# Performance work log

Measured on AMD Instinct MI355X. Metric: run time of the kernel, lower is better.

## Reference

```python
import jax, jax.numpy as jnp
import numpy as np
import math

H = 8
E = 512
D_K = E // H
NEG = -1000000000.0
# last (and only surviving) row of dist_bar: one threshold per head
DIST_BAR = np.array([0.2, 0.3, 0.4, 0.5, 0.6, 0.7, 0.8, 0.9], dtype=np.float32)


def setup_inputs() -> dict:
    key = jax.random.key(0)
    ks = jax.random.split(key, 12)
    B, N = 8, 1024
    s = 1.0 / math.sqrt(E)
    inp = {
        "query": jax.random.normal(ks[0], (B, N, E), jnp.float32),
        "key": jax.random.normal(ks[1], (B, N, E), jnp.float32),
        "value": jax.random.normal(ks[2], (B, N, E), jnp.float32),
        "dist": jax.random.uniform(ks[3], (B, 1, N, N), jnp.float32),
        "mask": jnp.ones((B, N, N), jnp.int32),
        "Wq": jax.random.normal(ks[4], (E, E), jnp.float32) * s,
        "bq": jnp.zeros((E,), jnp.float32),
        "Wk": jax.random.normal(ks[5], (E, E), jnp.float32) * s,
        "bk": jnp.zeros((E,), jnp.float32),
        "Wv": jax.random.normal(ks[6], (E, E), jnp.float32) * s,
        "bv": jnp.zeros((E,), jnp.float32),
        "Wo": jax.random.normal(ks[7], (E, E), jnp.float32) * s,
        "bo": jnp.zeros((E,), jnp.float32),
    }
    return inp


def reference(query, key, value, dist, mask, Wq, bq, Wk, bk, Wv, bv, Wo, bo):
    B, N, _ = query.shape
    # project and split heads: [B, H, N, D_K]
    def heads(x, W, b):
        return (x @ W.T + b).reshape(B, N, H, D_K).transpose(0, 2, 1, 3)
    q = heads(query, Wq, bq)
    k = heads(key, Wk, bk)
    v = heads(value, Wv, bv)
    scores = jnp.einsum("bhqd,bhkd->bhqk", q, k) / math.sqrt(D_K)
    # padding mask: [B,N,N] -> [B,1,N,N]
    scores = jnp.where(mask[:, None, :, :] == 0, NEG, scores)
    # per-head distance mask: dist [B,1,N,N] < thr[h] -> [B,H,N,N]
    thr = jnp.asarray(DIST_BAR)[None, :, None, None]
    dmask = dist < thr
    # first row/col (global atom) always attend
    dmask = dmask.at[:, :, 0, :].set(True).at[:, :, :, 0].set(True)
    scores = jnp.where(dmask, scores, NEG)
    p = jax.nn.softmax(scores, axis=-1)
    out = jnp.einsum("bhqk,bhkd->bhqd", p, v)  # [B,H,N,D_K]
    out = out.transpose(0, 2, 1, 3).reshape(B, N, H * D_K)
    return out @ Wo.T + bo
```

## Files before the change

kernel.cpp:

```cpp
#include <hip/hip_runtime.h>
#include <stdint.h>


typedef __attribute__((ext_vector_type(8))) short short8;
typedef __attribute__((ext_vector_type(4))) float floatx4;

#define MFMA16(a, b, c) __builtin_amdgcn_mfma_f32_16x16x32_bf16((a), (b), (c), 0, 0, 0)

static __device__ __forceinline__ unsigned short f2bf(float f) {
  union { float f; unsigned u; } v; v.f = f;
  unsigned r = v.u + 0x7fffu + ((v.u >> 16) & 1u);
  return (unsigned short)(r >> 16);
}

static __device__ __forceinline__ void gload_lds16(const void* g, void* l) {
  __builtin_amdgcn_global_load_lds((const __attribute__((address_space(1))) unsigned int*)g,
                                   (__attribute__((address_space(3))) unsigned int*)l,
                                   16, 0, 0);
}
static __device__ __forceinline__ int xsw(int row) { return (row & 3) ^ ((row >> 2) & 3); }

__global__ void wcast_kernel(const float* __restrict__ Wq, const float* __restrict__ Wk,
                             const float* __restrict__ Wv, const float* __restrict__ Wo,
                             unsigned short* __restrict__ o0, unsigned short* __restrict__ o1,
                             unsigned short* __restrict__ o2, unsigned short* __restrict__ o3) {
  int i = blockIdx.x * blockDim.x + threadIdx.x;
  int w = i >> 16, loc = i & 65535;
  const float* s = (w == 0) ? Wq : (w == 1) ? Wk : (w == 2) ? Wv : Wo;
  unsigned short* d = (w == 0) ? o0 : (w == 1) ? o1 : (w == 2) ? o2 : o3;
  float4 v = ((const float4*)s)[loc];
  ushort4 o;
  o.x = f2bf(v.x); o.y = f2bf(v.y); o.z = f2bf(v.z); o.w = f2bf(v.w);
  ((ushort4*)d)[loc] = o;
}

__global__ void codes_kernel(const float* __restrict__ dist, const int* __restrict__ mask,
                             unsigned char* __restrict__ codes) {
  int t = blockIdx.x * blockDim.x + threadIdx.x;
  int flat = t << 2;
  int rem = flat & ((1 << 20) - 1);
  int i = rem >> 10;
  int j0 = rem & 1023;
  float4 d4 = ((const float4*)dist)[t];
  int4 m4 = ((const int4*)mask)[t];
  float dv[4] = {d4.x, d4.y, d4.z, d4.w};
  int mv[4] = {m4.x, m4.y, m4.z, m4.w};
  unsigned char cv[4];
#pragma unroll
  for (int u = 0; u < 4; u++) {
    float d = dv[u];
    int hmin = (d >= 0.2f) + (d >= 0.3f) + (d >= 0.4f) + (d >= 0.5f) +
               (d >= 0.6f) + (d >= 0.7f) + (d >= 0.8f) + (d >= 0.9f);
    unsigned char cc = (unsigned char)hmin;
    if (i == 0 || (j0 + u) == 0) cc = 0;
    if (mv[u] == 0) cc = 9;
    cv[u] = cc;
  }
  uchar4 o; o.x = cv[0]; o.y = cv[1]; o.z = cv[2]; o.w = cv[3];
  ((uchar4*)codes)[t] = o;
}

__global__ __launch_bounds__(256) void qkv_gemm(
    const float* __restrict__ Aq, const float* __restrict__ Ak, const float* __restrict__ Av,
    const unsigned short* __restrict__ Wqp, const unsigned short* __restrict__ Wkp,
    const unsigned short* __restrict__ Wvp,
    const float* __restrict__ bq, const float* __restrict__ bk, const float* __restrict__ bv,
    unsigned short* __restrict__ Qh, unsigned short* __restrict__ Kh,
    unsigned short* __restrict__ Vt) {
  const int z = blockIdx.z;
  const float* A = (z == 0) ? Aq : (z == 1) ? Ak : Av;
  const unsigned short* W = (z == 0) ? Wqp : (z == 1) ? Wkp : Wvp;
  const float* bias = (z == 0) ? bq : (z == 1) ? bk : bv;
  unsigned short* O = (z == 0) ? Qh : (z == 1) ? Kh : Vt;

  __shared__ __align__(16) short As[64 * 40];
  __shared__ __align__(16) short Bs[128 * 32];
  const int tid = threadIdx.x;
  const int lane = tid & 63;
  const int wave = tid >> 6;
  const int c = lane & 15;
  const int q = lane >> 4;
  const int m0 = blockIdx.x * 64;
  const int n0 = blockIdx.y * 128;
  const int wr = (wave >> 1) * 32;
  const int wc = (wave & 1) * 64;

  floatx4 acc[2][4];
#pragma unroll
  for (int i = 0; i < 2; i++)
#pragma unroll
    for (int j = 0; j < 4; j++) acc[i][j] = (floatx4)(0.0f);

  const int arow = tid >> 2, ach = tid & 3;
  const float* Ab = A + (size_t)(m0 + arow) * 512 + ach * 8;

  for (int k0 = 0; k0 < 512; k0 += 32) {
    __syncthreads();
#pragma unroll
    for (int it = 0; it < 2; it++) {
      int slot = wave * 128 + it * 64 + lane;
      int brow = slot >> 2, bch = slot & 3;
      int g = bch ^ xsw(brow);
      gload_lds16(W + (size_t)(n0 + brow) * 512 + k0 + g * 8,
                  &Bs[(size_t)(wave * 128 + it * 64) * 8]);
    }
    float4 a0 = *(const float4*)(Ab + k0);
    float4 a1 = *(const float4*)(Ab + k0 + 4);
    short8 av;
    av[0] = (short)f2bf(a0.x); av[1] = (short)f2bf(a0.y);
    av[2] = (short)f2bf(a0.z); av[3] = (short)f2bf(a0.w);
    av[4] = (short)f2bf(a1.x); av[5] = (short)f2bf(a1.y);
    av[6] = (short)f2bf(a1.z); av[7] = (short)f2bf(a1.w);
    *(short8*)(&As[arow * 40 + ach * 8]) = av;
    __syncthreads();

    short8 af[2], bfv[4];
#pragma unroll
    for (int i = 0; i < 2; i++)
      af[i] = *(const short8*)(&As[(wr + i * 16 + c) * 40 + q * 8]);
#pragma unroll
    for (int j = 0; j < 4; j++) {
      int row = wc + j * 16 + c;
      bfv[j] = *(const short8*)(&Bs[row * 32 + (q ^ xsw(row)) * 8]);
    }
#pragma unroll
    for (int i = 0; i < 2; i++)
#pragma unroll
      for (int j = 0; j < 4; j++)
        acc[i][j] = MFMA16(af[i], bfv[j], acc[i][j]);
  }

#pragma unroll
  for (int i = 0; i < 2; i++) {
    int gm0 = m0 + wr + i * 16 + q * 4;
#pragma unroll
    for (int j = 0; j < 4; j++) {
      int gn = n0 + wc + j * 16 + c;
      float bb = bias[gn];
      int h = gn >> 6, d = gn & 63;
      if (z == 2) {
        int b = gm0 >> 10, n = gm0 & 1023;
        ushort4 pk;
#pragma unroll
        for (int r = 0; r < 4; r++) pk[r] = f2bf(acc[i][j][r] + bb);
        *(ushort4*)(&Vt[(((size_t)(b * 8 + h) * 64 + d) << 10) + n]) = pk;
      } else {
#pragma unroll
        for (int r = 0; r < 4; r++) {
          int m = gm0 + r;
          int b = m >> 10, n = m & 1023;
          O[((((size_t)(b * 8 + h)) << 10) + n) * 64 + d] = f2bf(acc[i][j][r] + bb);
        }
      }
    }
  }
}

__global__ __launch_bounds__(256) void out_gemm(const unsigned short* __restrict__ A,
                                                const unsigned short* __restrict__ W,
                                                const float* __restrict__ bias,
                                                float* __restrict__ Out) {
  __shared__ __align__(16) short As[64 * 32];
  __shared__ __align__(16) short Bs[128 * 32];
  const int tid = threadIdx.x;
  const int lane = tid & 63;
  const int wave = tid >> 6;
  const int c = lane & 15;
  const int q = lane >> 4;
  const int m0 = blockIdx.x * 64;
  const int n0 = blockIdx.y * 128;
  const int wr = (wave >> 1) * 32;
  const int wc = (wave & 1) * 64;

  floatx4 acc[2][4];
#pragma unroll
  for (int i = 0; i < 2; i++)
#pragma unroll
    for (int j = 0; j < 4; j++) acc[i][j] = (floatx4)(0.0f);

  for (int k0 = 0; k0 < 512; k0 += 32) {
    __syncthreads();
    {
      int slot = wave * 64 + lane;
      int arow = slot >> 2, ach = slot & 3;
      int g = ach ^ xsw(arow);
      gload_lds16(A + (size_t)(m0 + arow) * 512 + k0 + g * 8, &As[(size_t)(wave * 64) * 8]);
    }
#pragma unroll
    for (int it = 0; it < 2; it++) {
      int slot = wave * 128 + it * 64 + lane;
      int brow = slot >> 2, bch = slot & 3;
      int g = bch ^ xsw(brow);
      gload_lds16(W + (size_t)(n0 + brow) * 512 + k0 + g * 8,
                  &Bs[(size_t)(wave * 128 + it * 64) * 8]);
    }
    __syncthreads();

    short8 af[2], bfv[4];
#pragma unroll
    for (int i = 0; i < 2; i++) {
      int row = wr + i * 16 + c;
      af[i] = *(const short8*)(&As[row * 32 + (q ^ xsw(row)) * 8]);
    }
#pragma unroll
    for (int j = 0; j < 4; j++) {
      int row = wc + j * 16 + c;
      bfv[j] = *(const short8*)(&Bs[row * 32 + (q ^ xsw(row)) * 8]);
    }
#pragma unroll
    for (int i = 0; i < 2; i++)
#pragma unroll
      for (int j = 0; j < 4; j++)
        acc[i][j] = MFMA16(af[i], bfv[j], acc[i][j]);
  }

#pragma unroll
  for (int i = 0; i < 2; i++) {
    int gm0 = m0 + wr + i * 16 + q * 4;
#pragma unroll
    for (int j = 0; j < 4; j++) {
      int gn = n0 + wc + j * 16 + c;
      float bb = bias[gn];
#pragma unroll
      for (int r = 0; r < 4; r++)
        Out[(size_t)(gm0 + r) * 512 + gn] = acc[i][j][r] + bb;
    }
  }
}

__global__ __launch_bounds__(256) void attn_kernel(const unsigned short* __restrict__ Qh,
                                                   const unsigned short* __restrict__ Kh,
                                                   const unsigned short* __restrict__ Vt,
                                                   const unsigned char* __restrict__ codes,
                                                   unsigned short* __restrict__ AO) {
  __shared__ __align__(16) unsigned short P[32 * 136];
  __shared__ __align__(16) unsigned char Ct[32 * 128];
  __shared__ float S4[4][32];
  const int tid = threadIdx.x;
  const int lane = tid & 63;
  const int wave = tid >> 6;
  const int c = lane & 15;
  const int q = lane >> 4;
  const int qt = blockIdx.x;
  const int bh = blockIdx.y;
  const int b = bh >> 3;
  const int h = bh & 7;
  const size_t base = (size_t)bh << 16;
  const int ri = wave >> 1;
  const int dh = wave & 1;

  short8 aq[2][2];
#pragma unroll
  for (int qs = 0; qs < 2; qs++)
#pragma unroll
    for (int kk = 0; kk < 2; kk++)
      aq[qs][kk] = *(const short8*)(Qh + base + (size_t)(qt * 32 + qs * 16 + c) * 64 + kk * 32 + q * 8);

  const unsigned char* cbt = codes + ((size_t)b << 20) + ((size_t)(qt * 32 + (tid >> 3)) << 10) + (tid & 7) * 16;
  const unsigned short* Vb = Vt + base;

  float rs[2][4];
#pragma unroll
  for (int qs = 0; qs < 2; qs++)
#pragma unroll
    for (int r = 0; r < 4; r++) rs[qs][r] = 0.0f;
  floatx4 o[2];
  o[0] = (floatx4)(0.0f); o[1] = (floatx4)(0.0f);

  for (int kt = 0; kt < 8; kt++) {
    uint4 cw = *(const uint4*)(cbt + kt * 128);
    const int col0 = kt * 128 + wave * 32;
    floatx4 s[2][2];
#pragma unroll
    for (int qs = 0; qs < 2; qs++)
#pragma unroll
      for (int ci = 0; ci < 2; ci++) s[qs][ci] = (floatx4)(0.0f);
#pragma unroll
    for (int ci = 0; ci < 2; ci++)
#pragma unroll
      for (int kk = 0; kk < 2; kk++) {
        short8 bk = *(const short8*)(Kh + base + (size_t)(col0 + ci * 16 + c) * 64 + kk * 32 + q * 8);
        s[0][ci] = MFMA16(aq[0][kk], bk, s[0][ci]);
        s[1][ci] = MFMA16(aq[1][kk], bk, s[1][ci]);
      }
    *(uint4*)(&Ct[(tid >> 3) * 128 + (tid & 7) * 16]) = cw;
    __syncthreads();

#pragma unroll
    for (int qs = 0; qs < 2; qs++) {
      int rowb = qs * 16 + q * 4;
#pragma unroll
      for (int ci = 0; ci < 2; ci++) {
        int colw = wave * 32 + ci * 16 + c;
#pragma unroll
        for (int r = 0; r < 4; r++) {
          int row = rowb + r;
          unsigned char code = Ct[row * 128 + colw];
          float e = (h >= (int)code) ? exp2f(s[qs][ci][r] * 0.1803368801111362f) : 0.0f;
          rs[qs][r] += e;
          P[row * 136 + colw] = f2bf(e);
        }
      }
    }
    __syncthreads();

#pragma unroll
    for (int ch = 0; ch < 4; ch++) {
      short8 ap = *(const short8*)(&P[(ri * 16 + c) * 136 + ch * 32 + q * 8]);
      short8 bv0 = *(const short8*)(Vb + (size_t)(dh * 32 + c) * 1024 + kt * 128 + ch * 32 + q * 8);
      short8 bv1 = *(const short8*)(Vb + (size_t)(dh * 32 + 16 + c) * 1024 + kt * 128 + ch * 32 + q * 8);
      o[0] = MFMA16(ap, bv0, o[0]);
      o[1] = MFMA16(ap, bv1, o[1]);
    }
  }

#pragma unroll
  for (int qs = 0; qs < 2; qs++)
#pragma unroll
    for (int r = 0; r < 4; r++) {
      float v = rs[qs][r];
      v += __shfl_xor(v, 1); v += __shfl_xor(v, 2);
      v += __shfl_xor(v, 4); v += __shfl_xor(v, 8);
      rs[qs][r] = v;
    }
  if (c == 0) {
#pragma unroll
    for (int qs = 0; qs < 2; qs++)
#pragma unroll
      for (int r = 0; r < 4; r++) S4[wave][qs * 16 + q * 4 + r] = rs[qs][r];
  }
  __syncthreads();
  float inv[4];
#pragma unroll
  for (int r = 0; r < 4; r++) {
    int row = ri * 16 + q * 4 + r;
    inv[r] = 1.0f / (S4[0][row] + S4[1][row] + S4[2][row] + S4[3][row]);
  }
#pragma unroll
  for (int r = 0; r < 4; r++) {
    int ig = qt * 32 + ri * 16 + q * 4 + r;
    size_t ob = ((size_t)((b << 10) + ig)) * 512 + h * 64 + dh * 32;
    AO[ob + c] = f2bf(o[0][r] * inv[r]);
    AO[ob + 16 + c] = f2bf(o[1][r] * inv[r]);
  }
}

extern "C" void kernel_launch(void* const* d_in, const int* in_sizes, int n_in,
                              void* d_out, int out_size, void* d_ws, size_t ws_size,
                              hipStream_t stream) {
  const float* query = (const float*)d_in[0];
  const float* key_  = (const float*)d_in[1];
  const float* value = (const float*)d_in[2];
  const float* dist  = (const float*)d_in[3];
  const int*   mask  = (const int*)d_in[4];
  const float* Wq = (const float*)d_in[5];
  const float* bq = (const float*)d_in[6];
  const float* Wk = (const float*)d_in[7];
  const float* bk = (const float*)d_in[8];
  const float* Wv = (const float*)d_in[9];
  const float* bv = (const float*)d_in[10];
  const float* Wo = (const float*)d_in[11];
  const float* bo = (const float*)d_in[12];

  char* ws = (char*)d_ws;
  size_t off = 0;
  auto alloc = [&](size_t bytes) -> char* {
    char* p = ws + off;
    off += (bytes + 255) & ~(size_t)255;
    return p;
  };
  const size_t NQKV = 8192ull * 512;
  unsigned short* wq16 = (unsigned short*)alloc(512ull * 512 * 2);
  unsigned short* wk16 = (unsigned short*)alloc(512ull * 512 * 2);
  unsigned short* wv16 = (unsigned short*)alloc(512ull * 512 * 2);
  unsigned short* wo16 = (unsigned short*)alloc(512ull * 512 * 2);
  unsigned short* Qh = (unsigned short*)alloc(NQKV * 2);
  unsigned short* Kh = (unsigned short*)alloc(NQKV * 2);
  unsigned short* Vt = (unsigned short*)alloc(NQKV * 2);
  unsigned short* AO = (unsigned short*)alloc(NQKV * 2);
  unsigned char*  codes = (unsigned char*)alloc(8ull * 1024 * 1024);

  wcast_kernel<<<1024, 256, 0, stream>>>(Wq, Wk, Wv, Wo, wq16, wk16, wv16, wo16);
  codes_kernel<<<8192, 256, 0, stream>>>(dist, mask, codes);
  qkv_gemm<<<dim3(128, 4, 3), 256, 0, stream>>>(query, key_, value, wq16, wk16, wv16,
                                                bq, bk, bv, Qh, Kh, Vt);
  attn_kernel<<<dim3(32, 64), 256, 0, stream>>>(Qh, Kh, Vt, codes, AO);
  out_gemm<<<dim3(128, 4), 256, 0, stream>>>(AO, wo16, bo, (float*)d_out);
}
```

Measured before the change: 305.5 us.

## Give each wave its own query rows and pre-permute mask codes into MFMA lane layout

```diff
diff --git a/kernel.cpp b/kernel.cpp
--- a/kernel.cpp
+++ b/kernel.cpp
@@ -35,29 +35,36 @@
 }
 
 __global__ void codes_kernel(const float* __restrict__ dist, const int* __restrict__ mask,
-                             unsigned char* __restrict__ codes) {
+                             unsigned char* __restrict__ codesP) {
   int t = blockIdx.x * blockDim.x + threadIdx.x;
   int flat = t << 2;
+  int b = flat >> 20;
   int rem = flat & ((1 << 20) - 1);
-  int i = rem >> 10;
-  int j0 = rem & 1023;
+  int row = rem >> 10;
+  int col0 = rem & 1023;
   float4 d4 = ((const float4*)dist)[t];
   int4 m4 = ((const int4*)mask)[t];
   float dv[4] = {d4.x, d4.y, d4.z, d4.w};
   int mv[4] = {m4.x, m4.y, m4.z, m4.w};
-  unsigned char cv[4];
+  int rg = row >> 5;
+  int st = (row >> 4) & 1;
+  int qq = (row >> 2) & 3;
+  int r = row & 3;
+  size_t rowbase = (size_t)(b * 32 + rg) * 32768;
+  int sub = st * 32 + r;
 #pragma unroll
   for (int u = 0; u < 4; u++) {
+    int col = col0 + u;
     float d = dv[u];
     int hmin = (d >= 0.2f) + (d >= 0.3f) + (d >= 0.4f) + (d >= 0.5f) +
                (d >= 0.6f) + (d >= 0.7f) + (d >= 0.8f) + (d >= 0.9f);
     unsigned char cc = (unsigned char)hmin;
-    if (i == 0 || (j0 + u) == 0) cc = 0;
+    if (row == 0 || col == 0) cc = 0;
     if (mv[u] == 0) cc = 9;
-    cv[u] = cc;
-  }
-  uchar4 o; o.x = cv[0]; o.y = cv[1]; o.z = cv[2]; o.w = cv[3];
-  ((uchar4*)codes)[t] = o;
+    int kt = col >> 7, ci = (col >> 4) & 7, c = col & 15;
+    int lane = qq * 16 + c;
+    codesP[rowbase + (size_t)kt * 4096 + lane * 64 + sub + ci * 4] = cc;
+  }
 }
 
 __global__ __launch_bounds__(256) void qkv_gemm(
@@ -231,118 +238,109 @@
 __global__ __launch_bounds__(256) void attn_kernel(const unsigned short* __restrict__ Qh,
                                                    const unsigned short* __restrict__ Kh,
                                                    const unsigned short* __restrict__ Vt,
-                                                   const unsigned char* __restrict__ codes,
+                                                   const unsigned char* __restrict__ codesP,
                                                    unsigned short* __restrict__ AO) {
-  __shared__ __align__(16) unsigned short P[32 * 136];
-  __shared__ __align__(16) unsigned char Ct[32 * 128];
-  __shared__ float S4[4][32];
+  __shared__ __align__(16) unsigned short P[4][32 * 132];
   const int tid = threadIdx.x;
   const int lane = tid & 63;
   const int wave = tid >> 6;
   const int c = lane & 15;
   const int q = lane >> 4;
-  const int qt = blockIdx.x;
   const int bh = blockIdx.y;
   const int b = bh >> 3;
   const int h = bh & 7;
   const size_t base = (size_t)bh << 16;
-  const int ri = wave >> 1;
-  const int dh = wave & 1;
+  const int rbase = blockIdx.x * 128 + wave * 32;
+  const int rg = rbase >> 5;
+  unsigned short* Pw = &P[wave][0];
 
   short8 aq[2][2];
 #pragma unroll
-  for (int qs = 0; qs < 2; qs++)
+  for (int st = 0; st < 2; st++)
 #pragma unroll
     for (int kk = 0; kk < 2; kk++)
-      aq[qs][kk] = *(const short8*)(Qh + base + (size_t)(qt * 32 + qs * 16 + c) * 64 + kk * 32 + q * 8);
-
-  const unsigned char* cbt = codes + ((size_t)b << 20) + ((size_t)(qt * 32 + (tid >> 3)) << 10) + (tid & 7) * 16;
+      aq[st][kk] = *(const short8*)(Qh + base + (size_t)(rbase + st * 16 + c) * 64 + kk * 32 + q * 8);
+
+  const unsigned char* cbt = codesP + (size_t)(b * 32 + rg) * 32768 + lane * 64;
+  const unsigned short* Kb = Kh + base;
   const unsigned short* Vb = Vt + base;
 
   float rs[2][4];
 #pragma unroll
-  for (int qs = 0; qs < 2; qs++)
-#pragma unroll
-    for (int r = 0; r < 4; r++) rs[qs][r] = 0.0f;
-  floatx4 o[2];
-  o[0] = (floatx4)(0.0f); o[1] = (floatx4)(0.0f);
+  for (int st = 0; st < 2; st++)
+#pragma unroll
+    for (int r = 0; r < 4; r++) rs[st][r] = 0.0f;
+  floatx4 o[2][4];
+#pragma unroll
+  for (int st = 0; st < 2; st++)
+#pragma unroll
+    for (int ci = 0; ci < 4; ci++) o[st][ci] = (floatx4)(0.0f);
 
   for (int kt = 0; kt < 8; kt++) {
-    uint4 cw = *(const uint4*)(cbt + kt * 128);
-    const int col0 = kt * 128 + wave * 32;
-    floatx4 s[2][2];
-#pragma unroll
-    for (int qs = 0; qs < 2; qs++)
-#pragma unroll
-      for (int ci = 0; ci < 2; ci++) s[qs][ci] = (floatx4)(0.0f);
-#pragma unroll
-    for (int ci = 0; ci < 2; ci++)
+    const unsigned short* Kt = Kb + (size_t)kt * 128 * 64;
+    floatx4 s[2][8];
+#pragma unroll
+    for (int ci = 0; ci < 8; ci++) { s[0][ci] = (floatx4)(0.0f); s[1][ci] = (floatx4)(0.0f); }
+#pragma unroll
+    for (int ci = 0; ci < 8; ci++)
 #pragma unroll
       for (int kk = 0; kk < 2; kk++) {
-        short8 bk = *(const short8*)(Kh + base + (size_t)(col0 + ci * 16 + c) * 64 + kk * 32 + q * 8);
+        short8 bk = *(const short8*)(Kt + (size_t)(ci * 16 + c) * 64 + kk * 32 + q * 8);
         s[0][ci] = MFMA16(aq[0][kk], bk, s[0][ci]);
         s[1][ci] = MFMA16(aq[1][kk], bk, s[1][ci]);
       }
-    *(uint4*)(&Ct[(tid >> 3) * 128 + (tid & 7) * 16]) = cw;
-    __syncthreads();
-
-#pragma unroll
-    for (int qs = 0; qs < 2; qs++) {
-      int rowb = qs * 16 + q * 4;
-#pragma unroll
-      for (int ci = 0; ci < 2; ci++) {
-        int colw = wave * 32 + ci * 16 + c;
+    const unsigned char* cp = cbt + (size_t)kt * 4096;
+    uint4 w0 = *(const uint4*)(cp);
+    uint4 w1 = *(const uint4*)(cp + 16);
+    uint4 w2 = *(const uint4*)(cp + 32);
+    uint4 w3 = *(const uint4*)(cp + 48);
+    unsigned cv[16] = {w0.x, w0.y, w0.z, w0.w, w1.x, w1.y, w1.z, w1.w,
+                       w2.x, w2.y, w2.z, w2.w, w3.x, w3.y, w3.z, w3.w};
+#pragma unroll
+    for (int st = 0; st < 2; st++)
+#pragma unroll
+      for (int ci = 0; ci < 8; ci++)
 #pragma unroll
         for (int r = 0; r < 4; r++) {
-          int row = rowb + r;
-          unsigned char code = Ct[row * 128 + colw];
-          float e = (h >= (int)code) ? exp2f(s[qs][ci][r] * 0.1803368801111362f) : 0.0f;
-          rs[qs][r] += e;
-          P[row * 136 + colw] = f2bf(e);
+          int bidx = st * 32 + ci * 4 + r;
+          int code = (cv[bidx >> 2] >> ((bidx & 3) * 8)) & 0xff;
+          float e = (h >= code) ? exp2f(s[st][ci][r] * 0.1803368801111362f) : 0.0f;
+          rs[st][r] += e;
+          Pw[(st * 16 + q * 4 + r) * 132 + ci * 16 + c] = f2bf(e);
         }
+#pragma unroll
+    for (int ch = 0; ch < 4; ch++) {
+      short8 ap0 = *(const short8*)(&Pw[(size_t)c * 132 + ch * 32 + q * 8]);
+      short8 ap1 = *(const short8*)(&Pw[(size_t)(16 + c) * 132 + ch * 32 + q * 8]);
+#pragma unroll
+      for (int ci = 0; ci < 4; ci++) {
+        short8 bv = *(const short8*)(Vb + (size_t)(ci * 16 + c) * 1024 + kt * 128 + ch * 32 + q * 8);
+        o[0][ci] = MFMA16(ap0, bv, o[0][ci]);
+        o[1][ci] = MFMA16(ap1, bv, o[1][ci]);
       }
     }
-    __syncthreads();
-
-#pragma unroll
-    for (int ch = 0; ch < 4; ch++) {
-      short8 ap = *(const short8*)(&P[(ri * 16 + c) * 136 + ch * 32 + q * 8]);
-      short8 bv0 = *(const short8*)(Vb + (size_t)(dh * 32 + c) * 1024 + kt * 128 + ch * 32 + q * 8);
-      short8 bv1 = *(const short8*)(Vb + (size_t)(dh * 32 + 16 + c) * 1024 + kt * 128 + ch * 32 + q * 8);
-      o[0] = MFMA16(ap, bv0, o[0]);
-      o[1] = MFMA16(ap, bv1, o[1]);
-    }
-  }
-
-#pragma unroll
-  for (int qs = 0; qs < 2; qs++)
+  }
+
+  float inv[2][4];
+#pragma unroll
+  for (int st = 0; st < 2; st++)
 #pragma unroll
     for (int r = 0; r < 4; r++) {
-      float v = rs[qs][r];
+      float v = rs[st][r];
       v += __shfl_xor(v, 1); v += __shfl_xor(v, 2);
       v += __shfl_xor(v, 4); v += __shfl_xor(v, 8);
-      rs[qs][r] = v;
-    }
-  if (c == 0) {
-#pragma unroll
-    for (int qs = 0; qs < 2; qs++)
-#pragma unroll
-      for (int r = 0; r < 4; r++) S4[wave][qs * 16 + q * 4 + r] = rs[qs][r];
-  }
-  __syncthreads();
-  float inv[4];
-#pragma unroll
-  for (int r = 0; r < 4; r++) {
-    int row = ri * 16 + q * 4 + r;
-    inv[r] = 1.0f / (S4[0][row] + S4[1][row] + S4[2][row] + S4[3][row]);
-  }
-#pragma unroll
-  for (int r = 0; r < 4; r++) {
-    int ig = qt * 32 + ri * 16 + q * 4 + r;
-    size_t ob = ((size_t)((b << 10) + ig)) * 512 + h * 64 + dh * 32;
-    AO[ob + c] = f2bf(o[0][r] * inv[r]);
-    AO[ob + 16 + c] = f2bf(o[1][r] * inv[r]);
-  }
+      inv[st][r] = 1.0f / v;
+    }
+#pragma unroll
+  for (int st = 0; st < 2; st++)
+#pragma unroll
+    for (int r = 0; r < 4; r++) {
+      int n = rbase + st * 16 + q * 4 + r;
+      size_t ob = ((size_t)((b << 10) + n)) * 512 + h * 64;
+#pragma unroll
+      for (int ci = 0; ci < 4; ci++)
+        AO[ob + ci * 16 + c] = f2bf(o[st][ci][r] * inv[st][r]);
+    }
 }
 
 extern "C" void kernel_launch(void* const* d_in, const int* in_sizes, int n_in,
@@ -378,12 +376,12 @@
   unsigned short* Kh = (unsigned short*)alloc(NQKV * 2);
   unsigned short* Vt = (unsigned short*)alloc(NQKV * 2);
   unsigned short* AO = (unsigned short*)alloc(NQKV * 2);
-  unsigned char*  codes = (unsigned char*)alloc(8ull * 1024 * 1024);
+  unsigned char*  codesP = (unsigned char*)alloc(8ull * 1024 * 1024);
 
   wcast_kernel<<<1024, 256, 0, stream>>>(Wq, Wk, Wv, Wo, wq16, wk16, wv16, wo16);
-  codes_kernel<<<8192, 256, 0, stream>>>(dist, mask, codes);
+  codes_kernel<<<8192, 256, 0, stream>>>(dist, mask, codesP);
   qkv_gemm<<<dim3(128, 4, 3), 256, 0, stream>>>(query, key_, value, wq16, wk16, wv16,
                                                 bq, bk, bv, Qh, Kh, Vt);
-  attn_kernel<<<dim3(32, 64), 256, 0, stream>>>(Qh, Kh, Vt, codes, AO);
+  attn_kernel<<<dim3(8, 64), 256, 0, stream>>>(Qh, Kh, Vt, codesP, AO);
   out_gemm<<<dim3(128, 4), 256, 0, stream>>>(AO, wo16, bo, (float*)d_out);
 }
```

Result: faster. 292.8 us (-4.2%).
